# Performance work log

Measured on AMD Instinct MI355X. Metric: run time of the kernel, lower is better.

## Reference

```python
import jax, jax.numpy as jnp
import numpy as np

N = 50000
E = 800000
IN = 64
HID = 64
OUT = 32
R = 8
B = 8
EPS = 1e-5


def setup_inputs() -> dict:
    key = jax.random.key(0)
    ks = jax.random.split(key, 20)
    s_in = 1.0 / np.sqrt(IN)
    s_hid = 1.0 / np.sqrt(HID)
    inp = {
        "x": jax.random.normal(ks[0], (N, IN), dtype=jnp.float32),
        "edge_index": jax.random.randint(ks[1], (2, E), 0, N, dtype=jnp.int64) if jax.config.jax_enable_x64 else jax.random.randint(ks[1], (2, E), 0, N),
        "edge_type": jax.random.randint(ks[2], (E,), 0, R),
        # conv1: in -> hid
        "comp1": jax.random.normal(ks[3], (R, B), dtype=jnp.float32) * (1.0 / np.sqrt(B)),
        "bases1": jax.random.normal(ks[4], (B, IN, HID), dtype=jnp.float32) * s_in,
        "root1": jax.random.normal(ks[5], (IN, HID), dtype=jnp.float32) * s_in,
        "bias1": jnp.zeros((HID,), dtype=jnp.float32),
        # conv2 (hidden): hid -> hid
        "comp2": jax.random.normal(ks[6], (R, B), dtype=jnp.float32) * (1.0 / np.sqrt(B)),
        "bases2": jax.random.normal(ks[7], (B, HID, HID), dtype=jnp.float32) * s_hid,
        "root2": jax.random.normal(ks[8], (HID, HID), dtype=jnp.float32) * s_hid,
        "bias2": jnp.zeros((HID,), dtype=jnp.float32),
        # conv_out: hid -> out
        "comp3": jax.random.normal(ks[9], (R, B), dtype=jnp.float32) * (1.0 / np.sqrt(B)),
        "bases3": jax.random.normal(ks[10], (B, HID, OUT), dtype=jnp.float32) * s_hid,
        "root3": jax.random.normal(ks[11], (HID, OUT), dtype=jnp.float32) * s_hid,
        "bias3": jnp.zeros((OUT,), dtype=jnp.float32),
        # batchnorms
        "gamma1": jnp.ones((HID,), dtype=jnp.float32),
        "beta1": jnp.zeros((HID,), dtype=jnp.float32),
        "gamma2": jnp.ones((HID,), dtype=jnp.float32),
        "beta2": jnp.zeros((HID,), dtype=jnp.float32),
    }
    return inp


def rgcn_conv(x, src, dst, etype, comp, bases, root, bias):
    """PyG-style RGCNConv with basis decomposition and per-relation mean aggregation."""
    n = x.shape[0]
    # project node features through all bases: [N, B, O]
    xb = jnp.einsum('ni,bio->nbo', x, bases)
    # per-edge relation coefficients [E, B] contract with gathered basis features [E, B, O]
    msg = jnp.einsum('eb,ebo->eo', comp[etype], xb[src])
    # mean normalization per (dst node, relation)
    seg = dst * R + etype
    cnt = jax.ops.segment_sum(jnp.ones((msg.shape[0],), dtype=x.dtype), seg, num_segments=n * R)
    msg = msg / jnp.maximum(cnt[seg], 1.0)[:, None]
    agg = jax.ops.segment_sum(msg, dst, num_segments=n)
    return agg + x @ root + bias


def batch_norm(x, gamma, beta):
    mu = jnp.mean(x, axis=0)
    var = jnp.mean(jnp.square(x - mu), axis=0)  # biased, as torch BN training
    return (x - mu) * jax.lax.rsqrt(var + EPS) * gamma + beta


def reference(x, edge_index, edge_type, comp1, bases1, root1, bias1,
              comp2, bases2, root2, bias2, comp3, bases3, root3, bias3,
              gamma1, beta1, gamma2, beta2):
    src, dst = edge_index[0], edge_index[1]
    h = rgcn_conv(x, src, dst, edge_type, comp1, bases1, root1, bias1)
    h = batch_norm(jax.nn.relu(h), gamma1, beta1)  # dropout = identity (eval)
    h_res = h  # residual since in_channels == hidden_channels
    h2 = rgcn_conv(h, src, dst, edge_type, comp2, bases2, root2, bias2)
    h2 = batch_norm(jax.nn.relu(h2), gamma2, beta2)
    h = h2 + h_res
    out = rgcn_conv(h, src, dst, edge_type, comp3, bases3, root3, bias3)
    return out
```

## Files before the change

kernel.cpp:

```cpp
#include <hip/hip_runtime.h>

#define NN 50000
#define NE 800000
#define RR 8
#define BB 8
#define EPSV 1e-5f
#define SCAN_B ((NN + 255) / 256)
#define NGRP 64

typedef unsigned short bfu;
typedef signed char i8;
typedef __attribute__((ext_vector_type(8))) short bf16x8;
typedef __attribute__((ext_vector_type(4))) float f32x4;

__device__ inline float bf2f(bfu u) { return __uint_as_float(((unsigned)u) << 16); }
__device__ inline bfu f2bf(float f) {
    unsigned u = __float_as_uint(f);
    return (bfu)((u + 0x7fffu + ((u >> 16) & 1u)) >> 16);
}

#define NW1 36864L
#define NW2 36864L
#define NW3 18432L
#define NZ  (400000L + 50000L + 2L * NGRP * 128)

__device__ inline void build_one(const float* __restrict__ comp, const float* __restrict__ bases,
                                 const float* __restrict__ root, bfu* __restrict__ Wp,
                                 int O, int idx) {
    int k = idx / O, o = idx % O;
    float val;
    if (k < 512) {
        int r = k >> 6, i = k & 63;
        val = 0.f;
#pragma unroll
        for (int b = 0; b < BB; ++b)
            val += comp[r * BB + b] * bases[(b * 64 + i) * O + o];
    } else {
        val = root[(k - 512) * O + o];
    }
    int kt = k >> 5, kk = k & 31;
    int lane = ((kk >> 3) << 4) | (o & 15);
    int pos = ((kt * (O / 16) + (o >> 4)) * 64 + lane) * 8 + (kk & 7);
    Wp[pos] = f2bf(val);
}

__global__ void prep(const float* __restrict__ c1, const float* __restrict__ b1,
                     const float* __restrict__ r1, bfu* __restrict__ Wp1,
                     const float* __restrict__ c2, const float* __restrict__ b2,
                     const float* __restrict__ r2, bfu* __restrict__ Wp2,
                     const float* __restrict__ c3, const float* __restrict__ b3,
                     const float* __restrict__ r3, bfu* __restrict__ Wp3,
                     float* __restrict__ zbase) {
    long i = (long)blockIdx.x * blockDim.x + threadIdx.x;
    long stride = (long)gridDim.x * blockDim.x;
    const long tot = NW1 + NW2 + NW3 + NZ;
    for (; i < tot; i += stride) {
        if (i < NW1) build_one(c1, b1, r1, Wp1, 64, (int)i);
        else if (i < NW1 + NW2) build_one(c2, b2, r2, Wp2, 64, (int)(i - NW1));
        else if (i < NW1 + NW2 + NW3) build_one(c3, b3, r3, Wp3, 32, (int)(i - NW1 - NW2));
        else zbase[i - (NW1 + NW2 + NW3)] = 0.f;
    }
}

__global__ __launch_bounds__(256) void cvt_rows(const float* __restrict__ x,
                                                bfu* __restrict__ xb,
                                                i8* __restrict__ x8,
                                                float* __restrict__ xs) {
    int wv = threadIdx.x >> 6, lane = threadIdx.x & 63;
    int gw = blockIdx.x * 4 + wv, nw = gridDim.x * 4;
    for (int n = gw; n < NN; n += nw) {
        float v = x[(size_t)n * 64 + lane];
        xb[(size_t)n * 64 + lane] = f2bf(v);
        float am = fabsf(v);
#pragma unroll
        for (int d = 1; d < 64; d <<= 1) am = fmaxf(am, __shfl_xor(am, d));
        am = fmaxf(am, 1e-20f);
        float inv = 127.f / am;
        x8[(size_t)n * 64 + lane] = (i8)__float2int_rn(v * inv);
        if (lane == 0) xs[n] = am * (1.f / 127.f);
    }
}

__global__ void edge_count(const int* __restrict__ ei, const int* __restrict__ et,
                           float* __restrict__ cnt) {
    int range = blockIdx.x >> 8;
    int lo = range * (NN / 4), hi = lo + NN / 4;
    int i = (blockIdx.x & 255) * 256 + threadIdx.x;
    for (int e = i; e < NE; e += 256 * 256) {
        int d = ei[NE + e];
        if (d >= lo && d < hi)
            atomicAdd(&cnt[(size_t)d * RR + et[e]], 1.0f);
    }
}

__global__ void scan1(const float* __restrict__ cnt, int* __restrict__ offs, int* __restrict__ bsum) {
    __shared__ int sh[256];
    int b = blockIdx.x, t = threadIdx.x;
    int i = b * 256 + t;
    int v = 0;
    if (i < NN) {
        float s = 0.f;
#pragma unroll
        for (int r = 0; r < RR; ++r) s += cnt[(size_t)i * RR + r];
        v = (int)s;
    }
    sh[t] = v;
    __syncthreads();
    for (int s = 1; s < 256; s <<= 1) {
        int tmp = (t >= s) ? sh[t - s] : 0;
        __syncthreads();
        sh[t] += tmp;
        __syncthreads();
    }
    if (i < NN) offs[i] = sh[t] - v;
    if (t == 255) bsum[b] = sh[255];
}

__global__ void scan2(int* __restrict__ bsum, int* __restrict__ offs) {
    if (threadIdx.x == 0 && blockIdx.x == 0) {
        int run = 0;
        for (int b = 0; b < SCAN_B; ++b) { int t = bsum[b]; bsum[b] = run; run += t; }
        offs[NN] = run;
    }
}

__global__ void scan3(int* __restrict__ offs, const int* __restrict__ bsum) {
    int b = blockIdx.x, t = threadIdx.x;
    int i = b * 256 + t;
    if (i < NN) offs[i] += bsum[b];
}

__global__ void place(const int* __restrict__ ei, const int* __restrict__ et,
                      const int* __restrict__ offs, int* __restrict__ fill,
                      unsigned* __restrict__ esrt) {
    int range = blockIdx.x >> 8;
    int lo = range * (NN / 4), hi = lo + NN / 4;
    int i = (blockIdx.x & 255) * 256 + threadIdx.x;
    for (int e = i; e < NE; e += 256 * 256) {
        int d = ei[NE + e];
        if (d >= lo && d < hi) {
            int pos = offs[d] + atomicAdd(&fill[d], 1);
            esrt[pos] = ((unsigned)ei[e] << 3) | (unsigned)et[e];
        }
    }
}

#define ACCUMS(SU, V)                          \
    switch ((SU) & 7) {                        \
        case 0: a0 += (V); break;              \
        case 1: a1 += (V); break;              \
        case 2: a2 += (V); break;              \
        case 3: a3 += (V); break;              \
        case 4: a4 += (V); break;              \
        case 5: a5 += (V); break;              \
        case 6: a6 += (V); break;              \
        default: a7 += (V); break;             \
    }
#define RDL(X, L) __builtin_amdgcn_readlane((int)(X), (L))

template <int O, bool RELU, bool STATS>
__global__ __launch_bounds__(1024, 8) void agg_gemm(const int* __restrict__ offs,
                                                    const unsigned* __restrict__ esrt,
                                                    const float* __restrict__ cnt,
                                                    const i8* __restrict__ x8,
                                                    const float* __restrict__ xs,
                                                    const bfu* __restrict__ xb,
                                                    const bfu* __restrict__ Wp,
                                                    const float* __restrict__ bias,
                                                    float* __restrict__ outp,
                                                    float* __restrict__ stats) {
    constexpr int CT = O / 16;
    __shared__ bfu Af[1152 * 8];
    int wave = threadIdx.x >> 6, lane = threadIdx.x & 63;
    int n0 = blockIdx.x * 16;
    int row = wave;
    int n = n0 + row;
    int c = lane;
    int swz_lo = ((c >> 3) & 3) << 4;

    int j0 = offs[n], j1 = offs[n + 1];
    float a0 = 0.f, a1 = 0.f, a2 = 0.f, a3 = 0.f, a4 = 0.f, a5 = 0.f, a6 = 0.f, a7 = 0.f;
    int j = j0;
    unsigned mye = 0;
    if (j + 8 <= j1) mye = esrt[j + (lane & 7)];
    for (; j + 8 <= j1;) {
        unsigned cur = mye;
        float sc8 = xs[cur >> 3];
        int jn = j + 8;
        if (jn + 8 <= j1) mye = esrt[jn + (lane & 7)];
        int scb = __float_as_int(sc8);
        int s0 = RDL(cur, 0), s1 = RDL(cur, 1), s2 = RDL(cur, 2), s3 = RDL(cur, 3);
        int s4 = RDL(cur, 4), s5 = RDL(cur, 5), s6 = RDL(cur, 6), s7 = RDL(cur, 7);
        float q0 = (float)x8[(size_t)((unsigned)s0 >> 3) * 64 + lane];
        float q1 = (float)x8[(size_t)((unsigned)s1 >> 3) * 64 + lane];
        float q2 = (float)x8[(size_t)((unsigned)s2 >> 3) * 64 + lane];
        float q3 = (float)x8[(size_t)((unsigned)s3 >> 3) * 64 + lane];
        float q4 = (float)x8[(size_t)((unsigned)s4 >> 3) * 64 + lane];
        float q5 = (float)x8[(size_t)((unsigned)s5 >> 3) * 64 + lane];
        float q6 = (float)x8[(size_t)((unsigned)s6 >> 3) * 64 + lane];
        float q7 = (float)x8[(size_t)((unsigned)s7 >> 3) * 64 + lane];
        float c0 = __int_as_float(RDL(scb, 0)), c1 = __int_as_float(RDL(scb, 1));
        float c2 = __int_as_float(RDL(scb, 2)), c3 = __int_as_float(RDL(scb, 3));
        float c4 = __int_as_float(RDL(scb, 4)), c5 = __int_as_float(RDL(scb, 5));
        float c6 = __int_as_float(RDL(scb, 6)), c7 = __int_as_float(RDL(scb, 7));
        ACCUMS(s0, q0 * c0) ACCUMS(s1, q1 * c1) ACCUMS(s2, q2 * c2) ACCUMS(s3, q3 * c3)
        ACCUMS(s4, q4 * c4) ACCUMS(s5, q5 * c5) ACCUMS(s6, q6 * c6) ACCUMS(s7, q7 * c7)
        j = jn;
    }
    if (j + 4 <= j1) {
        unsigned m4 = esrt[j + (lane & 3)];
        float sc4 = xs[m4 >> 3];
        int scb = __float_as_int(sc4);
        int s0 = RDL(m4, 0), s1 = RDL(m4, 1), s2 = RDL(m4, 2), s3 = RDL(m4, 3);
        float q0 = (float)x8[(size_t)((unsigned)s0 >> 3) * 64 + lane];
        float q1 = (float)x8[(size_t)((unsigned)s1 >> 3) * 64 + lane];
        float q2 = (float)x8[(size_t)((unsigned)s2 >> 3) * 64 + lane];
        float q3 = (float)x8[(size_t)((unsigned)s3 >> 3) * 64 + lane];
        float c0 = __int_as_float(RDL(scb, 0)), c1 = __int_as_float(RDL(scb, 1));
        float c2 = __int_as_float(RDL(scb, 2)), c3 = __int_as_float(RDL(scb, 3));
        ACCUMS(s0, q0 * c0) ACCUMS(s1, q1 * c1) ACCUMS(s2, q2 * c2) ACCUMS(s3, q3 * c3)
        j += 4;
    }
    for (; j < j1; ++j) {
        int s0 = __builtin_amdgcn_readfirstlane((int)esrt[j]);
        float q0 = (float)x8[(size_t)((unsigned)s0 >> 3) * 64 + lane];
        float c0 = xs[(unsigned)s0 >> 3];
        ACCUMS(s0, q0 * c0)
    }
#define WR(r, ar) {                                                            \
    float inv = 1.f / fmaxf(cnt[(size_t)n * RR + (r)], 1.f);                   \
    bfu bv = f2bf((ar) * inv);                                                 \
    int g = (2 * (r) + (c >> 5)) * 64 + (row | swz_lo);                        \
    int gs = g ^ ((g >> 3) & 7) ^ ((g >> 6) & 7);                              \
    Af[gs * 8 + (c & 7)] = bv; }
    WR(0, a0) WR(1, a1) WR(2, a2) WR(3, a3)
    WR(4, a4) WR(5, a5) WR(6, a6) WR(7, a7)
#undef WR
    {
        bfu bv = xb[(size_t)n * 64 + lane];
        int g = (16 + (c >> 5)) * 64 + (row | swz_lo);
        int gs = g ^ ((g >> 3) & 7) ^ ((g >> 6) & 7);
        Af[gs * 8 + (c & 7)] = bv;
    }
    __syncthreads();

    int ct = wave;
    if (ct < CT) {
        f32x4 acc = (f32x4){0.f, 0.f, 0.f, 0.f};
#pragma unroll
        for (int kt = 0; kt < 18; ++kt) {
            int g = kt * 64 + lane;
            int gs = g ^ ((g >> 3) & 7) ^ ((g >> 6) & 7);
            bf16x8 af = *(const bf16x8*)&Af[gs * 8];
            bf16x8 bfv = *(const bf16x8*)&Wp[((size_t)(kt * CT + ct) * 64 + lane) * 8];
            acc = __builtin_amdgcn_mfma_f32_16x16x32_bf16(af, bfv, acc, 0, 0, 0);
        }
        int col = ct * 16 + (lane & 15);
        float b = bias[col];
        float ssum = 0.f, sq = 0.f;
#pragma unroll
        for (int jj = 0; jj < 4; ++jj) {
            int orow = (lane >> 4) * 4 + jj;
            float v = acc[jj] + b;
            if (RELU) v = fmaxf(v, 0.f);
            outp[(size_t)(n0 + orow) * O + col] = v;
            if (STATS) { ssum += v; sq += v * v; }
        }
        if (STATS) {
            ssum += __shfl_xor(ssum, 16); ssum += __shfl_xor(ssum, 32);
            sq   += __shfl_xor(sq, 16);   sq   += __shfl_xor(sq, 32);
            if ((lane >> 4) == 0) {
                int g = blockIdx.x & (NGRP - 1);
                atomicAdd(&stats[g * 128 + col], ssum);
                atomicAdd(&stats[g * 128 + 64 + col], sq);
            }
        }
    }
}

template <bool HASRES>
__global__ __launch_bounds__(256) void bn_apply(const float* __restrict__ y,
                                                const float* __restrict__ stats,
                                                const float* __restrict__ gamma,
                                                const float* __restrict__ beta,
                                                const bfu* __restrict__ resb,
                                                bfu* __restrict__ hb,
                                                i8* __restrict__ h8,
                                                float* __restrict__ hs) {
    __shared__ float sc[128];
    int t = threadIdx.x;
    if (t < 64) {
        float s = 0.f, q = 0.f;
        for (int g = 0; g < NGRP; ++g) {
            s += stats[g * 128 + t];
            q += stats[g * 128 + 64 + t];
        }
        float mu = s / (float)NN;
        float var = q / (float)NN - mu * mu;
        float scale = gamma[t] * rsqrtf(var + EPSV);
        sc[t] = scale;
        sc[64 + t] = beta[t] - mu * scale;
    }
    __syncthreads();
    int wv = threadIdx.x >> 6, lane = threadIdx.x & 63;
    int gw = blockIdx.x * 4 + wv, nw = gridDim.x * 4;
    for (int n = gw; n < NN; n += nw) {
        float v = y[(size_t)n * 64 + lane] * sc[lane] + sc[64 + lane];
        if (HASRES) v += bf2f(resb[(size_t)n * 64 + lane]);
        hb[(size_t)n * 64 + lane] = f2bf(v);
        float am = fabsf(v);
#pragma unroll
        for (int d = 1; d < 64; d <<= 1) am = fmaxf(am, __shfl_xor(am, d));
        am = fmaxf(am, 1e-20f);
        float inv = 127.f / am;
        h8[(size_t)n * 64 + lane] = (i8)__float2int_rn(v * inv);
        if (lane == 0) hs[n] = am * (1.f / 127.f);
    }
}

extern "C" void kernel_launch(void* const* d_in, const int* in_sizes, int n_in,
                              void* d_out, int out_size, void* d_ws, size_t ws_size,
                              hipStream_t stream) {
    const float* x      = (const float*)d_in[0];
    const int*   ei     = (const int*)d_in[1];
    const int*   et     = (const int*)d_in[2];
    const float* comp1  = (const float*)d_in[3];
    const float* bases1 = (const float*)d_in[4];
    const float* root1  = (const float*)d_in[5];
    const float* bias1  = (const float*)d_in[6];
    const float* comp2  = (const float*)d_in[7];
    const float* bases2 = (const float*)d_in[8];
    const float* root2  = (const float*)d_in[9];
    const float* bias2  = (const float*)d_in[10];
    const float* comp3  = (const float*)d_in[11];
    const float* bases3 = (const float*)d_in[12];
    const float* root3  = (const float*)d_in[13];
    const float* bias3  = (const float*)d_in[14];
    const float* gamma1 = (const float*)d_in[15];
    const float* beta1  = (const float*)d_in[16];
    const float* gamma2 = (const float*)d_in[17];
    const float* beta2  = (const float*)d_in[18];
    float* out = (float*)d_out;

    float* ws = (float*)d_ws;
    size_t off = 0;
    bfu* Wp1 = (bfu*)(ws + off); off += 18432;
    bfu* Wp2 = (bfu*)(ws + off); off += 18432;
    bfu* Wp3 = (bfu*)(ws + off); off += 9216;
    float* cnt    = ws + off; off += (size_t)NN * RR;
    int*   fill   = (int*)(ws + off); off += NN;
    float* stats1 = ws + off; off += NGRP * 128;
    float* stats2 = ws + off; off += NGRP * 128;
    float* y  = ws + off; off += (size_t)NN * 64;
    bfu* xb   = (bfu*)(ws + off); off += (size_t)NN * 32;
    bfu* h1b  = (bfu*)(ws + off); off += (size_t)NN * 32;
    bfu* hb   = (bfu*)(ws + off); off += (size_t)NN * 32;
    i8*  x8   = (i8*)(ws + off);  off += (size_t)NN * 16;
    i8*  h1_8 = (i8*)(ws + off);  off += (size_t)NN * 16;
    i8*  h_8  = (i8*)(ws + off);  off += (size_t)NN * 16;
    float* xsc  = ws + off; off += NN;
    float* h1sc = ws + off; off += NN;
    float* hsc  = ws + off; off += NN;
    int* offs = (int*)(ws + off); off += NN + 4;
    int* bsum = (int*)(ws + off); off += 256;
    unsigned* esrt = (unsigned*)(ws + off); off += NE;

    prep<<<dim3(1024), dim3(256), 0, stream>>>(comp1, bases1, root1, Wp1,
                                               comp2, bases2, root2, Wp2,
                                               comp3, bases3, root3, Wp3, cnt);
    cvt_rows<<<dim3(512), dim3(256), 0, stream>>>(x, xb, x8, xsc);
    edge_count<<<dim3(1024), dim3(256), 0, stream>>>(ei, et, cnt);
    scan1<<<dim3(SCAN_B), dim3(256), 0, stream>>>(cnt, offs, bsum);
    scan2<<<dim3(1), dim3(64), 0, stream>>>(bsum, offs);
    scan3<<<dim3(SCAN_B), dim3(256), 0, stream>>>(offs, bsum);
    place<<<dim3(1024), dim3(256), 0, stream>>>(ei, et, offs, fill, esrt);

    agg_gemm<64, true, true><<<dim3(NN / 16), dim3(1024), 0, stream>>>(offs, esrt, cnt, x8, xsc, xb, Wp1, bias1, y, stats1);
    bn_apply<false><<<dim3(1024), dim3(256), 0, stream>>>(y, stats1, gamma1, beta1, nullptr, h1b, h1_8, h1sc);

    agg_gemm<64, true, true><<<dim3(NN / 16), dim3(1024), 0, stream>>>(offs, esrt, cnt, h1_8, h1sc, h1b, Wp2, bias2, y, stats2);
    bn_apply<true><<<dim3(1024), dim3(256), 0, stream>>>(y, stats2, gamma2, beta2, h1b, hb, h_8, hsc);

    agg_gemm<32, false, false><<<dim3(NN / 16), dim3(1024), 0, stream>>>(offs, esrt, cnt, h_8, hsc, hb, Wp3, bias3, out, nullptr);
}
```

Before: 313.8 us.

## Sort nodes by in-degree to balance per-wave aggregation work in blocks

Builds a permutation of nodes ordered by descending in-degree using a histogram, scan and placement pass. Each aggregation block now processes 16 nodes of similar degree, and the output rows are scattered back through the permutation held in shared memory. This aims to cut idle waves waiting on the longest-degree node in a block and to schedule heavy blocks first. In exchange it adds three small kernels and makes output stores and row accesses non-contiguous.

```diff
diff --git a/kernel.cpp b/kernel.cpp
--- a/kernel.cpp
+++ b/kernel.cpp
@@ -22,7 +22,7 @@
 #define NW1 36864L
 #define NW2 36864L
 #define NW3 18432L
-#define NZ  (400000L + 50000L + 2L * NGRP * 128)
+#define NZ  (400000L + 50000L + 2L * NGRP * 128 + 256)
 
 __device__ inline void build_one(const float* __restrict__ comp, const float* __restrict__ bases,
                                  const float* __restrict__ root, bfu* __restrict__ Wp,
@@ -145,6 +145,34 @@
     }
 }
 
+__global__ void dhist(const int* __restrict__ offs, int* __restrict__ hist) {
+    int i = blockIdx.x * blockDim.x + threadIdx.x;
+    if (i < NN) {
+        int d = offs[i + 1] - offs[i]; if (d > 255) d = 255;
+        atomicAdd(&hist[255 - d], 1);
+    }
+}
+__global__ void dscan(int* __restrict__ hist) {
+    __shared__ int sh[256];
+    int t = threadIdx.x;
+    int v = hist[t]; sh[t] = v; __syncthreads();
+    for (int s = 1; s < 256; s <<= 1) {
+        int tmp = (t >= s) ? sh[t - s] : 0;
+        __syncthreads();
+        sh[t] += tmp;
+        __syncthreads();
+    }
+    hist[t] = sh[t] - v;
+}
+__global__ void dplace(const int* __restrict__ offs, int* __restrict__ hist, int* __restrict__ perm) {
+    int i = blockIdx.x * blockDim.x + threadIdx.x;
+    if (i < NN) {
+        int d = offs[i + 1] - offs[i]; if (d > 255) d = 255;
+        int slot = atomicAdd(&hist[255 - d], 1);
+        perm[slot] = i;
+    }
+}
+
 #define ACCUMS(SU, V)                          \
     switch ((SU) & 7) {                        \
         case 0: a0 += (V); break;              \
@@ -159,7 +187,8 @@
 #define RDL(X, L) __builtin_amdgcn_readlane((int)(X), (L))
 
 template <int O, bool RELU, bool STATS>
-__global__ __launch_bounds__(1024, 8) void agg_gemm(const int* __restrict__ offs,
+__global__ __launch_bounds__(1024, 8) void agg_gemm(const int* __restrict__ perm,
+                                                    const int* __restrict__ offs,
                                                     const unsigned* __restrict__ esrt,
                                                     const float* __restrict__ cnt,
                                                     const i8* __restrict__ x8,
@@ -171,10 +200,12 @@
                                                     float* __restrict__ stats) {
     constexpr int CT = O / 16;
     __shared__ bfu Af[1152 * 8];
+    __shared__ int permLds[16];
     int wave = threadIdx.x >> 6, lane = threadIdx.x & 63;
     int n0 = blockIdx.x * 16;
     int row = wave;
-    int n = n0 + row;
+    int n = perm[n0 + row];
+    if (lane == 0) permLds[row] = n;
     int c = lane;
     int swz_lo = ((c >> 3) & 3) << 4;
 
@@ -261,9 +292,10 @@
 #pragma unroll
         for (int jj = 0; jj < 4; ++jj) {
             int orow = (lane >> 4) * 4 + jj;
+            int pn = permLds[orow];
             float v = acc[jj] + b;
             if (RELU) v = fmaxf(v, 0.f);
-            outp[(size_t)(n0 + orow) * O + col] = v;
+            outp[(size_t)pn * O + col] = v;
             if (STATS) { ssum += v; sq += v * v; }
         }
         if (STATS) {
@@ -351,6 +383,7 @@
     int*   fill   = (int*)(ws + off); off += NN;
     float* stats1 = ws + off; off += NGRP * 128;
     float* stats2 = ws + off; off += NGRP * 128;
+    int*   hist   = (int*)(ws + off); off += 256;
     float* y  = ws + off; off += (size_t)NN * 64;
     bfu* xb   = (bfu*)(ws + off); off += (size_t)NN * 32;
     bfu* h1b  = (bfu*)(ws + off); off += (size_t)NN * 32;
@@ -363,6 +396,7 @@
     float* hsc  = ws + off; off += NN;
     int* offs = (int*)(ws + off); off += NN + 4;
     int* bsum = (int*)(ws + off); off += 256;
+    int* perm = (int*)(ws + off); off += NN;
     unsigned* esrt = (unsigned*)(ws + off); off += NE;
 
     prep<<<dim3(1024), dim3(256), 0, stream>>>(comp1, bases1, root1, Wp1,
@@ -374,12 +408,15 @@
     scan2<<<dim3(1), dim3(64), 0, stream>>>(bsum, offs);
     scan3<<<dim3(SCAN_B), dim3(256), 0, stream>>>(offs, bsum);
     place<<<dim3(1024), dim3(256), 0, stream>>>(ei, et, offs, fill, esrt);
-
-    agg_gemm<64, true, true><<<dim3(NN / 16), dim3(1024), 0, stream>>>(offs, esrt, cnt, x8, xsc, xb, Wp1, bias1, y, stats1);
+    dhist<<<dim3(SCAN_B), dim3(256), 0, stream>>>(offs, hist);
+    dscan<<<dim3(1), dim3(256), 0, stream>>>(hist);
+    dplace<<<dim3(SCAN_B), dim3(256), 0, stream>>>(offs, hist, perm);
+
+    agg_gemm<64, true, true><<<dim3(NN / 16), dim3(1024), 0, stream>>>(perm, offs, esrt, cnt, x8, xsc, xb, Wp1, bias1, y, stats1);
     bn_apply<false><<<dim3(1024), dim3(256), 0, stream>>>(y, stats1, gamma1, beta1, nullptr, h1b, h1_8, h1sc);
 
-    agg_gemm<64, true, true><<<dim3(NN / 16), dim3(1024), 0, stream>>>(offs, esrt, cnt, h1_8, h1sc, h1b, Wp2, bias2, y, stats2);
+    agg_gemm<64, true, true><<<dim3(NN / 16), dim3(1024), 0, stream>>>(perm, offs, esrt, cnt, h1_8, h1sc, h1b, Wp2, bias2, y, stats2);
     bn_apply<true><<<dim3(1024), dim3(256), 0, stream>>>(y, stats2, gamma2, beta2, h1b, hb, h_8, hsc);
 
-    agg_gemm<32, false, false><<<dim3(NN / 16), dim3(1024), 0, stream>>>(offs, esrt, cnt, h_8, hsc, hb, Wp3, bias3, out, nullptr);
-}
+    agg_gemm<32, false, false><<<dim3(NN / 16), dim3(1024), 0, stream>>>(perm, offs, esrt, cnt, h_8, hsc, hb, Wp3, bias3, out, nullptr);
+}
```

New measurement: 526.7 us. 67.9% more time.

## Sort edges by (dst, relation) to aggregate per relation segment without switches

Applied to the files above, without the earlier changes.

Edges are now sorted into per-(destination, relation) segments through a new per-key offset kernel and keyed atomic fill, so each relation's sum runs as a contiguous loop with one accumulator. This removes the per-edge switch dispatch over eight accumulators and the packed relation bits. In exchange there are eight small segment loops per node with poor 4-wide batching (about 2 edges per relation on average), more scalar tail iterations, an extra kernel, and larger fill/offset arrays with more atomic contention spread.

```diff
diff --git a/kernel.cpp b/kernel.cpp
--- a/kernel.cpp
+++ b/kernel.cpp
@@ -22,7 +22,7 @@
 #define NW1 36864L
 #define NW2 36864L
 #define NW3 18432L
-#define NZ  (400000L + 50000L + 2L * NGRP * 128)
+#define NZ  (400000L + 400000L + 2L * NGRP * 128)
 
 __device__ inline void build_one(const float* __restrict__ comp, const float* __restrict__ bases,
                                  const float* __restrict__ root, bfu* __restrict__ Wp,
@@ -130,8 +130,21 @@
     if (i < NN) offs[i] += bsum[b];
 }
 
+__global__ void offs2k(const int* __restrict__ offs, const float* __restrict__ cnt,
+                       int* __restrict__ offs2) {
+    int n = blockIdx.x * blockDim.x + threadIdx.x;
+    if (n < NN) {
+        int base = offs[n];
+#pragma unroll
+        for (int r = 0; r < RR; ++r) {
+            offs2[n * RR + r] = base;
+            base += (int)cnt[(size_t)n * RR + r];
+        }
+    }
+}
+
 __global__ void place(const int* __restrict__ ei, const int* __restrict__ et,
-                      const int* __restrict__ offs, int* __restrict__ fill,
+                      const int* __restrict__ offs2, int* __restrict__ fill2,
                       unsigned* __restrict__ esrt) {
     int range = blockIdx.x >> 8;
     int lo = range * (NN / 4), hi = lo + NN / 4;
@@ -139,24 +152,40 @@
     for (int e = i; e < NE; e += 256 * 256) {
         int d = ei[NE + e];
         if (d >= lo && d < hi) {
-            int pos = offs[d] + atomicAdd(&fill[d], 1);
-            esrt[pos] = ((unsigned)ei[e] << 3) | (unsigned)et[e];
-        }
-    }
-}
-
-#define ACCUMS(SU, V)                          \
-    switch ((SU) & 7) {                        \
-        case 0: a0 += (V); break;              \
-        case 1: a1 += (V); break;              \
-        case 2: a2 += (V); break;              \
-        case 3: a3 += (V); break;              \
-        case 4: a4 += (V); break;              \
-        case 5: a5 += (V); break;              \
-        case 6: a6 += (V); break;              \
-        default: a7 += (V); break;             \
-    }
+            int key = d * RR + et[e];
+            int pos = offs2[key] + atomicAdd(&fill2[key], 1);
+            esrt[pos] = (unsigned)ei[e];
+        }
+    }
+}
+
 #define RDL(X, L) __builtin_amdgcn_readlane((int)(X), (L))
+
+#define SEG(rr, ar) {                                                           \
+    int len = (int)crow[rr];                                                    \
+    int je = jb + len;                                                          \
+    float a = 0.f;                                                              \
+    int j = jb;                                                                 \
+    for (; j + 4 <= je; j += 4) {                                               \
+        unsigned m4 = esrt[j + (lane & 3)];                                     \
+        float scl = xs[m4];                                                     \
+        int scb = __float_as_int(scl);                                          \
+        int s0 = RDL(m4, 0), s1 = RDL(m4, 1), s2 = RDL(m4, 2), s3 = RDL(m4, 3); \
+        float q0 = (float)x8[(size_t)(unsigned)s0 * 64 + lane];                 \
+        float q1 = (float)x8[(size_t)(unsigned)s1 * 64 + lane];                 \
+        float q2 = (float)x8[(size_t)(unsigned)s2 * 64 + lane];                 \
+        float q3 = (float)x8[(size_t)(unsigned)s3 * 64 + lane];                 \
+        a += q0 * __int_as_float(RDL(scb, 0));                                  \
+        a += q1 * __int_as_float(RDL(scb, 1));                                  \
+        a += q2 * __int_as_float(RDL(scb, 2));                                  \
+        a += q3 * __int_as_float(RDL(scb, 3));                                  \
+    }                                                                           \
+    for (; j < je; ++j) {                                                       \
+        int s0 = __builtin_amdgcn_readfirstlane((int)esrt[j]);                  \
+        a += (float)x8[(size_t)(unsigned)s0 * 64 + lane] * xs[(unsigned)s0];    \
+    }                                                                           \
+    jb = je;                                                                    \
+    ar = a / fmaxf((float)len, 1.f); }
 
 template <int O, bool RELU, bool STATS>
 __global__ __launch_bounds__(1024, 8) void agg_gemm(const int* __restrict__ offs,
@@ -178,58 +207,14 @@
     int c = lane;
     int swz_lo = ((c >> 3) & 3) << 4;
 
-    int j0 = offs[n], j1 = offs[n + 1];
-    float a0 = 0.f, a1 = 0.f, a2 = 0.f, a3 = 0.f, a4 = 0.f, a5 = 0.f, a6 = 0.f, a7 = 0.f;
-    int j = j0;
-    unsigned mye = 0;
-    if (j + 8 <= j1) mye = esrt[j + (lane & 7)];
-    for (; j + 8 <= j1;) {
-        unsigned cur = mye;
-        float sc8 = xs[cur >> 3];
-        int jn = j + 8;
-        if (jn + 8 <= j1) mye = esrt[jn + (lane & 7)];
-        int scb = __float_as_int(sc8);
-        int s0 = RDL(cur, 0), s1 = RDL(cur, 1), s2 = RDL(cur, 2), s3 = RDL(cur, 3);
-        int s4 = RDL(cur, 4), s5 = RDL(cur, 5), s6 = RDL(cur, 6), s7 = RDL(cur, 7);
-        float q0 = (float)x8[(size_t)((unsigned)s0 >> 3) * 64 + lane];
-        float q1 = (float)x8[(size_t)((unsigned)s1 >> 3) * 64 + lane];
-        float q2 = (float)x8[(size_t)((unsigned)s2 >> 3) * 64 + lane];
-        float q3 = (float)x8[(size_t)((unsigned)s3 >> 3) * 64 + lane];
-        float q4 = (float)x8[(size_t)((unsigned)s4 >> 3) * 64 + lane];
-        float q5 = (float)x8[(size_t)((unsigned)s5 >> 3) * 64 + lane];
-        float q6 = (float)x8[(size_t)((unsigned)s6 >> 3) * 64 + lane];
-        float q7 = (float)x8[(size_t)((unsigned)s7 >> 3) * 64 + lane];
-        float c0 = __int_as_float(RDL(scb, 0)), c1 = __int_as_float(RDL(scb, 1));
-        float c2 = __int_as_float(RDL(scb, 2)), c3 = __int_as_float(RDL(scb, 3));
-        float c4 = __int_as_float(RDL(scb, 4)), c5 = __int_as_float(RDL(scb, 5));
-        float c6 = __int_as_float(RDL(scb, 6)), c7 = __int_as_float(RDL(scb, 7));
-        ACCUMS(s0, q0 * c0) ACCUMS(s1, q1 * c1) ACCUMS(s2, q2 * c2) ACCUMS(s3, q3 * c3)
-        ACCUMS(s4, q4 * c4) ACCUMS(s5, q5 * c5) ACCUMS(s6, q6 * c6) ACCUMS(s7, q7 * c7)
-        j = jn;
-    }
-    if (j + 4 <= j1) {
-        unsigned m4 = esrt[j + (lane & 3)];
-        float sc4 = xs[m4 >> 3];
-        int scb = __float_as_int(sc4);
-        int s0 = RDL(m4, 0), s1 = RDL(m4, 1), s2 = RDL(m4, 2), s3 = RDL(m4, 3);
-        float q0 = (float)x8[(size_t)((unsigned)s0 >> 3) * 64 + lane];
-        float q1 = (float)x8[(size_t)((unsigned)s1 >> 3) * 64 + lane];
-        float q2 = (float)x8[(size_t)((unsigned)s2 >> 3) * 64 + lane];
-        float q3 = (float)x8[(size_t)((unsigned)s3 >> 3) * 64 + lane];
-        float c0 = __int_as_float(RDL(scb, 0)), c1 = __int_as_float(RDL(scb, 1));
-        float c2 = __int_as_float(RDL(scb, 2)), c3 = __int_as_float(RDL(scb, 3));
-        ACCUMS(s0, q0 * c0) ACCUMS(s1, q1 * c1) ACCUMS(s2, q2 * c2) ACCUMS(s3, q3 * c3)
-        j += 4;
-    }
-    for (; j < j1; ++j) {
-        int s0 = __builtin_amdgcn_readfirstlane((int)esrt[j]);
-        float q0 = (float)x8[(size_t)((unsigned)s0 >> 3) * 64 + lane];
-        float c0 = xs[(unsigned)s0 >> 3];
-        ACCUMS(s0, q0 * c0)
-    }
+    const float* crow = &cnt[(size_t)n * RR];
+    int jb = offs[n];
+    float a0, a1, a2, a3, a4, a5, a6, a7;
+    SEG(0, a0) SEG(1, a1) SEG(2, a2) SEG(3, a3)
+    SEG(4, a4) SEG(5, a5) SEG(6, a6) SEG(7, a7)
+
 #define WR(r, ar) {                                                            \
-    float inv = 1.f / fmaxf(cnt[(size_t)n * RR + (r)], 1.f);                   \
-    bfu bv = f2bf((ar) * inv);                                                 \
+    bfu bv = f2bf(ar);                                                         \
     int g = (2 * (r) + (c >> 5)) * 64 + (row | swz_lo);                        \
     int gs = g ^ ((g >> 3) & 7) ^ ((g >> 6) & 7);                              \
     Af[gs * 8 + (c & 7)] = bv; }
@@ -348,7 +333,7 @@
     bfu* Wp2 = (bfu*)(ws + off); off += 18432;
     bfu* Wp3 = (bfu*)(ws + off); off += 9216;
     float* cnt    = ws + off; off += (size_t)NN * RR;
-    int*   fill   = (int*)(ws + off); off += NN;
+    int*   fill2  = (int*)(ws + off); off += (size_t)NN * RR;
     float* stats1 = ws + off; off += NGRP * 128;
     float* stats2 = ws + off; off += NGRP * 128;
     float* y  = ws + off; off += (size_t)NN * 64;
@@ -361,8 +346,9 @@
     float* xsc  = ws + off; off += NN;
     float* h1sc = ws + off; off += NN;
     float* hsc  = ws + off; off += NN;
-    int* offs = (int*)(ws + off); off += NN + 4;
-    int* bsum = (int*)(ws + off); off += 256;
+    int* offs  = (int*)(ws + off); off += NN + 4;
+    int* bsum  = (int*)(ws + off); off += 256;
+    int* offs2 = (int*)(ws + off); off += (size_t)NN * RR;
     unsigned* esrt = (unsigned*)(ws + off); off += NE;
 
     prep<<<dim3(1024), dim3(256), 0, stream>>>(comp1, bases1, root1, Wp1,
@@ -373,7 +359,8 @@
     scan1<<<dim3(SCAN_B), dim3(256), 0, stream>>>(cnt, offs, bsum);
     scan2<<<dim3(1), dim3(64), 0, stream>>>(bsum, offs);
     scan3<<<dim3(SCAN_B), dim3(256), 0, stream>>>(offs, bsum);
-    place<<<dim3(1024), dim3(256), 0, stream>>>(ei, et, offs, fill, esrt);
+    offs2k<<<dim3(SCAN_B), dim3(256), 0, stream>>>(offs, cnt, offs2);
+    place<<<dim3(1024), dim3(256), 0, stream>>>(ei, et, offs2, fill2, esrt);
 
     agg_gemm<64, true, true><<<dim3(NN / 16), dim3(1024), 0, stream>>>(offs, esrt, cnt, x8, xsc, xb, Wp1, bias1, y, stats1);
     bn_apply<false><<<dim3(1024), dim3(256), 0, stream>>>(y, stats1, gamma1, beta1, nullptr, h1b, h1_8, h1sc);
```

Measured after the change: 395.7 us. 26.1% more time.
